# Kernel optimization log

Measured on AMD Instinct MI355X. Metric: run time of the kernel, lower is better.

The kernel has to match this reference:

```python
import jax, jax.numpy as jnp
import numpy as np

EPS = 1e-12  # F.normalize eps


def _gather_nb(var, idx):
    # var: [B, N, C], idx: [B, N, K] -> [B, N, K, C]; out[b,n,k,c] = var[b, idx[b,n,k], c]
    return jnp.take_along_axis(var[:, :, None, :], idx[:, :, :, None], axis=1)


def _l2norm(v):
    n = jnp.sqrt(jnp.sum(v * v, axis=-1, keepdims=True))
    return v / jnp.maximum(n, EPS)


def setup_inputs() -> dict:
    key = jax.random.key(0)
    ks = jax.random.split(key, 16)
    B, N, K, dim, hid = 4, 4096, 16, 128, 64
    s = 0.05
    return {
        "pos": jax.random.normal(ks[0], (B, N, 3), jnp.float32),
        "x": jax.random.normal(ks[1], (B, dim, N), jnp.float32),
        "idx": jax.random.randint(ks[2], (B, N, K), 0, N, jnp.int64),
        "dist": jax.random.uniform(ks[3], (B, N, K), jnp.float32),
        "W_qkv": jax.random.normal(ks[4], (3 * dim, dim), jnp.float32) * s,
        "W1": jax.random.normal(ks[5], (hid, 10), jnp.float32) * s,
        "b1": jax.random.normal(ks[6], (hid,), jnp.float32) * s,
        "W2": jax.random.normal(ks[7], (dim, hid), jnp.float32) * s,
        "b2": jax.random.normal(ks[8], (dim,), jnp.float32) * s,
        "Wm1": jax.random.normal(ks[9], (4 * dim, dim), jnp.float32) * s,
        "bm1": jax.random.normal(ks[10], (4 * dim,), jnp.float32) * s,
        "Wm2": jax.random.normal(ks[11], (dim, 4 * dim), jnp.float32) * s,
        "bm2": jax.random.normal(ks[12], (dim,), jnp.float32) * s,
    }


def reference(pos, x, idx, dist, W_qkv, W1, b1, W2, b2, Wm1, bm1, Wm2, bm2):
    B, _, N = x.shape
    xt = jnp.transpose(x, (0, 2, 1))                      # [B, N, C]
    qkv = xt @ W_qkv.T                                    # [B, N, 3C]
    Q, K_, V = jnp.split(qkv, 3, axis=-1)

    Qg = _gather_nb(Q, idx)                               # [B, N, K, C]
    Kg = _gather_nb(K_, idx)
    Vg = _gather_nb(V, idx)

    # position embedding: [center(3) | neighbor(3) | diff(3) | dist(1)] -> MLP 10->hid->C
    pos_nb = _gather_nb(pos, idx)                         # [B, N, K, 3]
    pos_c = jnp.broadcast_to(pos[:, :, None, :], pos_nb.shape)
    feat10 = jnp.concatenate(
        [pos_c, pos_nb, pos_c - pos_nb, dist[..., None]], axis=-1)  # [B, N, K, 10]
    pos_emb = jax.nn.relu(feat10 @ W1.T + b1) @ W2.T + b2  # [B, N, K, C]

    Knorm = _l2norm(Kg + pos_emb)                         # [B, N, K, C]
    Vrel = jax.nn.relu(Vg + pos_emb)                      # [B, N, K, C]
    Qn = _l2norm(Qg)                                      # [B, N, K, C]

    # kv_context: contract over N per neighbor slot k -> [B, K, C, C]
    kv = jnp.einsum('bnkc,bnkd->bkcd', Knorm, Vrel)
    # (1/N) Qn @ kv, then sum over k -> [B, N, C]
    agg = jnp.einsum('bnkc,bkcd->bnd', Qn, kv) / N

    out = jax.nn.relu(agg @ Wm1.T + bm1) @ Wm2.T + bm2 + xt  # [B, N, C]
    return jnp.transpose(out, (0, 2, 1))                     # [B, C, N]
```

## Files before the change

### kernel.cpp

```cpp
#include <hip/hip_runtime.h>
#include <math.h>

#define Bn 4
#define Nn 4096
#define Kn 16
#define Cn 128
#define HIDn 64

#define OFF_WQKVBF 0
#define OFF_WM1BF  24576
#define OFF_WM2BF  57344
#define OFF_W2BFG  90112
#define OFF_QNBF   95232
#define OFF_KMBF   1143808
#define OFF_VMBF   2192384
#define OFF_KVT32  3240960
#define OFF_KVTBF  4289536
#define OFF_AGG0   4813824
#define OFF_AGG1   6910976
#define OFF_FLAG   9008128

typedef short bf16x8 __attribute__((ext_vector_type(8)));
typedef float f32x4 __attribute__((ext_vector_type(4)));

__device__ inline unsigned short f2bf(float f) {
  union { float f; unsigned u; } v; v.f = f;
  unsigned r = v.u + 0x7fffu + ((v.u >> 16) & 1u);
  return (unsigned short)(r >> 16);
}
__device__ inline float b2f(unsigned short s) {
  union { unsigned u; float f; } v; v.u = ((unsigned)s) << 16; return v.f;
}

__global__ void k0_prep(const float* __restrict__ Wqkv,
                        const float* __restrict__ Wm1, const float* __restrict__ Wm2,
                        const float* __restrict__ W2,
                        const int* __restrict__ idx_raw, float* ws) {
  if (blockIdx.x == 0 && threadIdx.x == 0) {
    int any = 0;
    for (int i = 0; i < 64; ++i) any |= idx_raw[2 * i + 1];
    ((int*)(ws + OFF_FLAG))[0] = (any == 0) ? 1 : 0;
  }
  int t = blockIdx.x * 256 + threadIdx.x;
  if (t < 49152) { ((unsigned short*)(ws + OFF_WQKVBF))[t] = f2bf(Wqkv[t]); return; }
  t -= 49152;
  if (t < 65536) { ((unsigned short*)(ws + OFF_WM1BF))[t] = f2bf(Wm1[t]); return; }
  t -= 65536;
  if (t < 65536) { ((unsigned short*)(ws + OFF_WM2BF))[t] = f2bf(Wm2[t]); return; }
  t -= 65536;
  if (t < 8192) { ((unsigned short*)(ws + OFF_W2BFG))[t] = f2bf(W2[t]); return; }
}

__global__ __launch_bounds__(256, 2) void k1_qkv(const float* __restrict__ x, float* ws) {
  __shared__ __align__(16) unsigned short a_lds[32 * 136];
  __shared__ __align__(16) float qkv_lds[32 * 388];
  const unsigned short* Wq = (const unsigned short*)(ws + OFF_WQKVBF);
  unsigned short* Qnbf = (unsigned short*)(ws + OFF_QNBF);
  unsigned short* KmBF = (unsigned short*)(ws + OFF_KMBF);
  unsigned short* VmBF = (unsigned short*)(ws + OFF_VMBF);
  int b = blockIdx.x >> 7;
  int n0 = (blockIdx.x & 127) << 5;
  int t = threadIdx.x;
  int w = t >> 6, l = t & 63, ml = l & 15, gq = l >> 4;
#pragma unroll
  for (int i = 0; i < 16; ++i) {
    int id = t + 256 * i;
    int c = id >> 5, j = id & 31;
    a_lds[j * 136 + c] = f2bf(x[(b * Cn + c) * Nn + n0 + j]);
  }
  __syncthreads();
  f32x4 acc[2][6];
#pragma unroll
  for (int i = 0; i < 2; ++i)
#pragma unroll
    for (int j = 0; j < 6; ++j) acc[i][j] = (f32x4)0.f;
#pragma unroll
  for (int kc = 0; kc < 4; ++kc) {
    bf16x8 av0 = *(const bf16x8*)&a_lds[ml * 136 + kc * 32 + 8 * gq];
    bf16x8 av1 = *(const bf16x8*)&a_lds[(ml + 16) * 136 + kc * 32 + 8 * gq];
#pragma unroll
    for (int nf = 0; nf < 6; ++nf) {
      int m = 96 * w + 16 * nf + ml;
      bf16x8 bv = *(const bf16x8*)&Wq[m * 128 + kc * 32 + 8 * gq];
      acc[0][nf] = __builtin_amdgcn_mfma_f32_16x16x32_bf16(av0, bv, acc[0][nf], 0, 0, 0);
      acc[1][nf] = __builtin_amdgcn_mfma_f32_16x16x32_bf16(av1, bv, acc[1][nf], 0, 0, 0);
    }
  }
#pragma unroll
  for (int mf = 0; mf < 2; ++mf)
#pragma unroll
    for (int nf = 0; nf < 6; ++nf)
#pragma unroll
      for (int r = 0; r < 4; ++r)
        qkv_lds[(16 * mf + 4 * gq + r) * 388 + 96 * w + 16 * nf + ml] = acc[mf][nf][r];
  __syncthreads();
  {
    int g = t >> 3, l8 = t & 7;
    float4 q4[4];
    float ss = 0.f;
#pragma unroll
    for (int q = 0; q < 4; ++q) {
      q4[q] = *(const float4*)&qkv_lds[g * 388 + l8 * 16 + 4 * q];
      ss = fmaf(q4[q].x, q4[q].x, ss); ss = fmaf(q4[q].y, q4[q].y, ss);
      ss = fmaf(q4[q].z, q4[q].z, ss); ss = fmaf(q4[q].w, q4[q].w, ss);
    }
    ss += __shfl_xor(ss, 1); ss += __shfl_xor(ss, 2); ss += __shfl_xor(ss, 4);
    float sc = 1.f / fmaxf(sqrtf(ss), 1e-12f);
    union { unsigned short us[8]; uint4 u4; } o0, o1;
#pragma unroll
    for (int q = 0; q < 2; ++q) {
      o0.us[q * 4 + 0] = f2bf(q4[q].x * sc); o0.us[q * 4 + 1] = f2bf(q4[q].y * sc);
      o0.us[q * 4 + 2] = f2bf(q4[q].z * sc); o0.us[q * 4 + 3] = f2bf(q4[q].w * sc);
    }
#pragma unroll
    for (int q = 0; q < 2; ++q) {
      o1.us[q * 4 + 0] = f2bf(q4[2 + q].x * sc); o1.us[q * 4 + 1] = f2bf(q4[2 + q].y * sc);
      o1.us[q * 4 + 2] = f2bf(q4[2 + q].z * sc); o1.us[q * 4 + 3] = f2bf(q4[2 + q].w * sc);
    }
    *(uint4*)&Qnbf[(b * Nn + n0 + g) * Cn + l8 * 16] = o0.u4;
    *(uint4*)&Qnbf[(b * Nn + n0 + g) * Cn + l8 * 16 + 8] = o1.u4;
  }
#pragma unroll
  for (int i = 0; i < 2; ++i) {
    int id = t + 256 * i;
    int row = id >> 4, c8 = id & 15;
    const float* kp = &qkv_lds[row * 388 + 128 + c8 * 8];
    const float* vp = &qkv_lds[row * 388 + 256 + c8 * 8];
    union { unsigned short us[8]; uint4 u4; } ko, vo;
#pragma unroll
    for (int j = 0; j < 8; ++j) { ko.us[j] = f2bf(kp[j]); vo.us[j] = f2bf(vp[j]); }
    *(uint4*)&KmBF[(b * Nn + n0 + row) * Cn + c8 * 8] = ko.u4;
    *(uint4*)&VmBF[(b * Nn + n0 + row) * Cn + c8 * 8] = vo.u4;
  }
}

#define CH2 8
__global__ __launch_bounds__(256, 2) void k2_kv(const float* __restrict__ pos,
                                                const float* __restrict__ dist,
                                                const int* __restrict__ idxp,
                                                const float* __restrict__ W1,
                                                const float* __restrict__ b1,
                                                const float* __restrict__ b2,
                                                float* ws) {
  __shared__ __align__(16) unsigned short h_lds[32 * 72];
  __shared__ __align__(16) unsigned short pe_bf[32 * 136];
  __shared__ __align__(16) unsigned short K_rm[32 * 136];
  __shared__ __align__(16) unsigned short V_rm[32 * 136];
  __shared__ __align__(16) unsigned short KnT[2][128 * 40];
  __shared__ __align__(16) unsigned short VrT[2][128 * 40];

  const unsigned short* KmBF = (const unsigned short*)(ws + OFF_KMBF);
  const unsigned short* VmBF = (const unsigned short*)(ws + OFF_VMBF);
  const unsigned short* W2g = (const unsigned short*)(ws + OFF_W2BFG);
  float* kvt = ws + OFF_KVT32;
  int flag = ((const int*)(ws + OFF_FLAG))[0];

  int bid = blockIdx.x;
  int b = bid & 3;
  int rest = bid >> 2;
  int k = rest & 15, ch = rest >> 4;
  int t = threadIdx.x;
  int w = t >> 6, l = t & 63;
  int ml = l & 15, gq = l >> 4;

  int g = t >> 3, l8 = t & 7;
  int nl = (t >> 3) & 7, half = t & 7;
  int n_b2 = 8 * w + nl;
  int side = t >> 7, cc = t & 127;

  float b2v0 = b2[32 * w + ml];
  float b2v1 = b2[32 * w + 16 + ml];

  f32x4 acc[2][8];
#pragma unroll
  for (int i = 0; i < 2; ++i)
#pragma unroll
    for (int j = 0; j < 8; ++j) acc[i][j] = (f32x4)0.f;

  int nbase = ch * 512;
  union U8 { unsigned short us[8]; uint4 u4; };

  int fidx_m = (b * Nn + nbase + g) * Kn + k;
  int jn_m = flag ? idxp[2 * fidx_m] : idxp[fidx_m];
  float dd = dist[fidx_m];
  float pc0 = pos[(b * Nn + nbase + g) * 3 + 0];
  float pc1 = pos[(b * Nn + nbase + g) * 3 + 1];
  float pc2 = pos[(b * Nn + nbase + g) * 3 + 2];
  float pn0 = pos[(b * Nn + jn_m) * 3 + 0];
  float pn1 = pos[(b * Nn + jn_m) * 3 + 1];
  float pn2 = pos[(b * Nn + jn_m) * 3 + 2];
  int fidx_b = (b * Nn + nbase + n_b2) * Kn + k;
  int jn_b = flag ? idxp[2 * fidx_b] : idxp[fidx_b];
  U8 ka, kb, va, vb;
  {
    const unsigned short* krow = &KmBF[(b * Nn + jn_b) * Cn];
    const unsigned short* vrow = &VmBF[(b * Nn + jn_b) * Cn];
    ka.u4 = *(const uint4*)&krow[half * 16];
    kb.u4 = *(const uint4*)&krow[half * 16 + 8];
    va.u4 = *(const uint4*)&vrow[half * 16];
    vb.u4 = *(const uint4*)&vrow[half * 16 + 8];
  }

  for (int it = 0; it < 16; ++it) {
    {
      float f10[10] = {pc0, pc1, pc2, pn0, pn1, pn2, pc0 - pn0, pc1 - pn1, pc2 - pn2, dd};
      union { unsigned short us[8]; uint4 u4; } hv;
#pragma unroll
      for (int oo = 0; oo < 8; ++oo) {
        int o = l8 * 8 + oo;
        float a = b1[o];
#pragma unroll
        for (int i2 = 0; i2 < 10; ++i2) a = fmaf(W1[o * 10 + i2], f10[i2], a);
        hv.us[oo] = f2bf(fmaxf(a, 0.f));
      }
      *(uint4*)&h_lds[g * 72 + l8 * 8] = hv.u4;
    }
    int itn = (it < 15) ? it + 1 : 15;
    int n0n = nbase + itn * 32;
    int fidx_mn = (b * Nn + n0n + g) * Kn + k;
    int jn_mn = flag ? idxp[2 * fidx_mn] : idxp[fidx_mn];
    float ddn = dist[fidx_mn];
    int fidx_bn = (b * Nn + n0n + n_b2) * Kn + k;
    int jn_bn = flag ? idxp[2 * fidx_bn] : idxp[fidx_bn];
    __syncthreads();
    if (it > 0) {
      const unsigned short* ktp = KnT[(it - 1) & 1];
      const unsigned short* vtp = VrT[(it - 1) & 1];
      bf16x8 av[2];
#pragma unroll
      for (int mf = 0; mf < 2; ++mf)
        av[mf] = *(const bf16x8*)&vtp[(32 * w + 16 * mf + ml) * 40 + 8 * gq];
#pragma unroll
      for (int nf = 0; nf < 8; ++nf) {
        bf16x8 bv = *(const bf16x8*)&ktp[(16 * nf + ml) * 40 + 8 * gq];
#pragma unroll
        for (int mf = 0; mf < 2; ++mf)
          acc[mf][nf] = __builtin_amdgcn_mfma_f32_16x16x32_bf16(av[mf], bv, acc[mf][nf], 0, 0, 0);
      }
    }
    {
      f32x4 pacc[2][2];
#pragma unroll
      for (int i = 0; i < 2; ++i)
#pragma unroll
        for (int j = 0; j < 2; ++j) pacc[i][j] = (f32x4)0.f;
#pragma unroll
      for (int hc = 0; hc < 64; hc += 32) {
        bf16x8 av[2];
#pragma unroll
        for (int mf = 0; mf < 2; ++mf)
          av[mf] = *(const bf16x8*)&h_lds[(ml + 16 * mf) * 72 + hc + 8 * gq];
#pragma unroll
        for (int nf = 0; nf < 2; ++nf) {
          int c = 32 * w + 16 * nf + ml;
          bf16x8 bv = *(const bf16x8*)&W2g[c * 64 + hc + 8 * gq];
          pacc[0][nf] = __builtin_amdgcn_mfma_f32_16x16x32_bf16(av[0], bv, pacc[0][nf], 0, 0, 0);
          pacc[1][nf] = __builtin_amdgcn_mfma_f32_16x16x32_bf16(av[1], bv, pacc[1][nf], 0, 0, 0);
        }
      }
#pragma unroll
      for (int mf = 0; mf < 2; ++mf)
#pragma unroll
        for (int nf = 0; nf < 2; ++nf) {
          int c = 32 * w + 16 * nf + ml;
          float bias = nf ? b2v1 : b2v0;
#pragma unroll
          for (int r = 0; r < 4; ++r)
            pe_bf[(16 * mf + 4 * gq + r) * 136 + c] = f2bf(pacc[mf][nf][r] + bias);
        }
    }
    __syncthreads();
    {
      U8 pa, pb;
      pa.u4 = *(const uint4*)&pe_bf[n_b2 * 136 + half * 16];
      pb.u4 = *(const uint4*)&pe_bf[n_b2 * 136 + half * 16 + 8];
      float kr[16], vr[16];
      float ss = 0.f;
#pragma unroll
      for (int j = 0; j < 16; ++j) {
        float pe = b2f((j < 8) ? pa.us[j] : pb.us[j - 8]);
        float kg = b2f((j < 8) ? ka.us[j] : kb.us[j - 8]);
        float vg = b2f((j < 8) ? va.us[j] : vb.us[j - 8]);
        kr[j] = kg + pe;
        vr[j] = fmaxf(vg + pe, 0.f);
        ss = fmaf(kr[j], kr[j], ss);
      }
      ss += __shfl_xor(ss, 1); ss += __shfl_xor(ss, 2); ss += __shfl_xor(ss, 4);
      float sc = 1.f / fmaxf(sqrtf(ss), 1e-12f);
      union { unsigned short us[8]; uint4 u4; } o;
#pragma unroll
      for (int hh = 0; hh < 2; ++hh) {
#pragma unroll
        for (int j = 0; j < 8; ++j) o.us[j] = f2bf(kr[hh * 8 + j] * sc);
        *(uint4*)&K_rm[n_b2 * 136 + half * 16 + 8 * hh] = o.u4;
      }
#pragma unroll
      for (int hh = 0; hh < 2; ++hh) {
#pragma unroll
        for (int j = 0; j < 8; ++j) o.us[j] = f2bf(vr[hh * 8 + j]);
        *(uint4*)&V_rm[n_b2 * 136 + half * 16 + 8 * hh] = o.u4;
      }
    }
    float pc0n = pos[(b * Nn + n0n + g) * 3 + 0];
    float pc1n = pos[(b * Nn + n0n + g) * 3 + 1];
    float pc2n = pos[(b * Nn + n0n + g) * 3 + 2];
    float pn0n = pos[(b * Nn + jn_mn) * 3 + 0];
    float pn1n = pos[(b * Nn + jn_mn) * 3 + 1];
    float pn2n = pos[(b * Nn + jn_mn) * 3 + 2];
    U8 kan, kbn, van, vbn;
    {
      const unsigned short* krow = &KmBF[(b * Nn + jn_bn) * Cn];
      const unsigned short* vrow = &VmBF[(b * Nn + jn_bn) * Cn];
      kan.u4 = *(const uint4*)&krow[half * 16];
      kbn.u4 = *(const uint4*)&krow[half * 16 + 8];
      van.u4 = *(const uint4*)&vrow[half * 16];
      vbn.u4 = *(const uint4*)&vrow[half * 16 + 8];
    }
    __syncthreads();
    {
      const unsigned short* src = side ? V_rm : K_rm;
      unsigned short* dst = side ? VrT[it & 1] : KnT[it & 1];
      unsigned v[16];
#pragma unroll
      for (int i = 0; i < 16; ++i) {
        unsigned lo = src[(2 * i) * 136 + cc];
        unsigned hi = src[(2 * i + 1) * 136 + cc];
        v[i] = lo | (hi << 16);
      }
#pragma unroll
      for (int i = 0; i < 4; ++i) {
        uint4 pk = {v[4 * i], v[4 * i + 1], v[4 * i + 2], v[4 * i + 3]};
        *(uint4*)&dst[cc * 40 + 8 * i] = pk;
      }
    }
    dd = ddn;
    pc0 = pc0n; pc1 = pc1n; pc2 = pc2n;
    pn0 = pn0n; pn1 = pn1n; pn2 = pn2n;
    ka.u4 = kan.u4; kb.u4 = kbn.u4; va.u4 = van.u4; vb.u4 = vbn.u4;
  }
  __syncthreads();
  {
    const unsigned short* ktp = KnT[15 & 1];
    const unsigned short* vtp = VrT[15 & 1];
    bf16x8 av[2];
#pragma unroll
    for (int mf = 0; mf < 2; ++mf)
      av[mf] = *(const bf16x8*)&vtp[(32 * w + 16 * mf + ml) * 40 + 8 * gq];
#pragma unroll
    for (int nf = 0; nf < 8; ++nf) {
      bf16x8 bv = *(const bf16x8*)&ktp[(16 * nf + ml) * 40 + 8 * gq];
#pragma unroll
      for (int mf = 0; mf < 2; ++mf)
        acc[mf][nf] = __builtin_amdgcn_mfma_f32_16x16x32_bf16(av[mf], bv, acc[mf][nf], 0, 0, 0);
    }
  }
  float* kvp = kvt + (b * Kn + k) * Cn * Cn;
#pragma unroll
  for (int mf = 0; mf < 2; ++mf)
#pragma unroll
    for (int nf = 0; nf < 8; ++nf) {
      int c = 16 * nf + ml;
#pragma unroll
      for (int r = 0; r < 4; ++r) {
        int d = 32 * w + 16 * mf + 4 * gq + r;
        atomicAdd(&kvp[d * Cn + c], acc[mf][nf][r]);
      }
    }
}

__global__ __launch_bounds__(256) void k2b_cvt(float* ws) {
  const float* src = ws + OFF_KVT32;
  unsigned short* dst = (unsigned short*)(ws + OFF_KVTBF);
  int i = blockIdx.x * 256 + threadIdx.x;
  float4 a = *(const float4*)&src[i * 8];
  float4 c = *(const float4*)&src[i * 8 + 4];
  union { unsigned short us[8]; uint4 u4; } o;
  o.us[0] = f2bf(a.x); o.us[1] = f2bf(a.y); o.us[2] = f2bf(a.z); o.us[3] = f2bf(a.w);
  o.us[4] = f2bf(c.x); o.us[5] = f2bf(c.y); o.us[6] = f2bf(c.z); o.us[7] = f2bf(c.w);
  *(uint4*)&dst[i * 8] = o.u4;
}

__global__ __launch_bounds__(256, 4) void k3_agg(const int* __restrict__ idxp, float* ws) {
  __shared__ __align__(16) unsigned short qt[32 * 136];
  const unsigned short* Qnbf = (const unsigned short*)(ws + OFF_QNBF);
  const unsigned short* kvtbf = (const unsigned short*)(ws + OFF_KVTBF);
  int flag = ((const int*)(ws + OFF_FLAG))[0];

  int bid = blockIdx.x;
  int b = bid & 3;
  int kh = (bid >> 2) & 1;
  int nt = bid >> 3;
  int n0 = nt * 32;
  int t = threadIdx.x;
  int w = t >> 6, l = t & 63;
  int ml = l & 15, gq = l >> 4;

  f32x4 acc[2][2];
#pragma unroll
  for (int i = 0; i < 2; ++i)
#pragma unroll
    for (int j = 0; j < 2; ++j) acc[i][j] = (f32x4)0.f;

  for (int kk = 0; kk < 8; ++kk) {
    int k = kh * 8 + kk;
    __syncthreads();
#pragma unroll
    for (int i = 0; i < 2; ++i) {
      int id = t + 256 * i;
      int row = id >> 4, c16 = id & 15;
      int fidx = (b * Nn + n0 + row) * Kn + k;
      int jn = flag ? idxp[2 * fidx] : idxp[fidx];
      uint4 v = *(const uint4*)&Qnbf[(b * Nn + jn) * Cn + c16 * 8];
      *(uint4*)&qt[row * 136 + c16 * 8] = v;
    }
    __syncthreads();
    const unsigned short* kvp = &kvtbf[(b * Kn + k) * Cn * Cn];
#pragma unroll
    for (int c0 = 0; c0 < 128; c0 += 32) {
      bf16x8 a0 = *(const bf16x8*)&qt[ml * 136 + c0 + 8 * gq];
      bf16x8 a1 = *(const bf16x8*)&qt[(ml + 16) * 136 + c0 + 8 * gq];
#pragma unroll
      for (int nf = 0; nf < 2; ++nf) {
        int d = 32 * w + 16 * nf + ml;
        bf16x8 bv = *(const bf16x8*)&kvp[d * Cn + c0 + 8 * gq];
        acc[0][nf] = __builtin_amdgcn_mfma_f32_16x16x32_bf16(a0, bv, acc[0][nf], 0, 0, 0);
        acc[1][nf] = __builtin_amdgcn_mfma_f32_16x16x32_bf16(a1, bv, acc[1][nf], 0, 0, 0);
      }
    }
  }
  float* ag = ws + (kh ? OFF_AGG1 : OFF_AGG0);
#pragma unroll
  for (int mf = 0; mf < 2; ++mf)
#pragma unroll
    for (int nf = 0; nf < 2; ++nf) {
      int d = 32 * w + 16 * nf + ml;
#pragma unroll
      for (int r = 0; r < 4; ++r) {
        int n = n0 + 16 * mf + 4 * gq + r;
        ag[(b * Nn + n) * Cn + d] = acc[mf][nf][r];
      }
    }
}

__global__ __launch_bounds__(256, 2) void k4_mlp(const float* __restrict__ x,
                                                 const float* __restrict__ bm1,
                                                 const float* __restrict__ bm2,
                                                 float* __restrict__ out, float* ws) {
  __shared__ __align__(16) unsigned short a_lds[32 * 136];
  __shared__ __align__(16) unsigned short h_lds[32 * 520];
  __shared__ float out_s[128 * 33];
  const float* agg0 = ws + OFF_AGG0;
  const float* agg1 = ws + OFF_AGG1;
  const unsigned short* Wm1bf = (const unsigned short*)(ws + OFF_WM1BF);
  const unsigned short* Wm2bf = (const unsigned short*)(ws + OFF_WM2BF);
  const float invN = 1.f / (float)Nn;
  int b = blockIdx.x >> 7;
  int n0 = (blockIdx.x & 127) << 5;
  int t = threadIdx.x;
  int w = t >> 6, l = t & 63, ml = l & 15, gq = l >> 4;
#pragma unroll
  for (int i = 0; i < 4; ++i) {
    int id = t + 256 * i;
    int row = id >> 5, c4 = id & 31;
    int off = (b * Nn + n0 + row) * Cn + c4 * 4;
    float4 v0 = *(const float4*)&agg0[off];
    float4 v1 = *(const float4*)&agg1[off];
    union { unsigned short us[4]; uint2 u2; } o;
    o.us[0] = f2bf((v0.x + v1.x) * invN); o.us[1] = f2bf((v0.y + v1.y) * invN);
    o.us[2] = f2bf((v0.z + v1.z) * invN); o.us[3] = f2bf((v0.w + v1.w) * invN);
    *(uint2*)&a_lds[row * 136 + c4 * 4] = o.u2;
  }
  __syncthreads();
  {
    f32x4 hacc[2][8];
#pragma unroll
    for (int i = 0; i < 2; ++i)
#pragma unroll
      for (int j = 0; j < 8; ++j) hacc[i][j] = (f32x4)0.f;
#pragma unroll
    for (int kc = 0; kc < 4; ++kc) {
      bf16x8 av0 = *(const bf16x8*)&a_lds[ml * 136 + kc * 32 + 8 * gq];
      bf16x8 av1 = *(const bf16x8*)&a_lds[(ml + 16) * 136 + kc * 32 + 8 * gq];
#pragma unroll
      for (int nf = 0; nf < 8; ++nf) {
        int h = 128 * w + 16 * nf + ml;
        bf16x8 bv = *(const bf16x8*)&Wm1bf[h * 128 + kc * 32 + 8 * gq];
        hacc[0][nf] = __builtin_amdgcn_mfma_f32_16x16x32_bf16(av0, bv, hacc[0][nf], 0, 0, 0);
        hacc[1][nf] = __builtin_amdgcn_mfma_f32_16x16x32_bf16(av1, bv, hacc[1][nf], 0, 0, 0);
      }
    }
#pragma unroll
    for (int mf = 0; mf < 2; ++mf)
#pragma unroll
      for (int nf = 0; nf < 8; ++nf) {
        int h = 128 * w + 16 * nf + ml;
        float bias = bm1[h];
#pragma unroll
        for (int r = 0; r < 4; ++r)
          h_lds[(16 * mf + 4 * gq + r) * 520 + h] = f2bf(fmaxf(hacc[mf][nf][r] + bias, 0.f));
      }
  }
  __syncthreads();
  {
    f32x4 oacc[2][2];
#pragma unroll
    for (int i = 0; i < 2; ++i)
#pragma unroll
      for (int j = 0; j < 2; ++j) oacc[i][j] = (f32x4)0.f;
#pragma unroll
    for (int kc = 0; kc < 16; ++kc) {
      bf16x8 av0 = *(const bf16x8*)&h_lds[ml * 520 + kc * 32 + 8 * gq];
      bf16x8 av1 = *(const bf16x8*)&h_lds[(ml + 16) * 520 + kc * 32 + 8 * gq];
#pragma unroll
      for (int nf = 0; nf < 2; ++nf) {
        int co = 32 * w + 16 * nf + ml;
        bf16x8 bv = *(const bf16x8*)&Wm2bf[co * 512 + kc * 32 + 8 * gq];
        oacc[0][nf] = __builtin_amdgcn_mfma_f32_16x16x32_bf16(av0, bv, oacc[0][nf], 0, 0, 0);
        oacc[1][nf] = __builtin_amdgcn_mfma_f32_16x16x32_bf16(av1, bv, oacc[1][nf], 0, 0, 0);
      }
    }
#pragma unroll
    for (int mf = 0; mf < 2; ++mf)
#pragma unroll
      for (int nf = 0; nf < 2; ++nf) {
        int co = 32 * w + 16 * nf + ml;
        float bias = bm2[co];
#pragma unroll
        for (int r = 0; r < 4; ++r)
          out_s[co * 33 + 16 * mf + 4 * gq + r] = oacc[mf][nf][r] + bias;
      }
  }
  __syncthreads();
#pragma unroll
  for (int i = 0; i < 16; ++i) {
    int id = t + 256 * i;
    int co = id >> 5, j = id & 31;
    out[(b * Cn + co) * Nn + n0 + j] = out_s[co * 33 + j] + x[(b * Cn + co) * Nn + n0 + j];
  }
}

extern "C" void kernel_launch(void* const* d_in, const int* in_sizes, int n_in,
                              void* d_out, int out_size, void* d_ws, size_t ws_size,
                              hipStream_t stream) {
  const float* pos  = (const float*)d_in[0];
  const float* x    = (const float*)d_in[1];
  const int*   idx  = (const int*)d_in[2];
  const float* dist = (const float*)d_in[3];
  const float* Wqkv = (const float*)d_in[4];
  const float* W1   = (const float*)d_in[5];
  const float* b1   = (const float*)d_in[6];
  const float* W2   = (const float*)d_in[7];
  const float* b2   = (const float*)d_in[8];
  const float* Wm1  = (const float*)d_in[9];
  const float* bm1  = (const float*)d_in[10];
  const float* Wm2  = (const float*)d_in[11];
  const float* bm2  = (const float*)d_in[12];
  float* out = (float*)d_out;
  float* ws = (float*)d_ws;

  hipMemsetAsync(ws + OFF_KVT32, 0, (size_t)Bn * Kn * Cn * Cn * sizeof(float), stream);
  hipLaunchKernelGGL(k0_prep, dim3(736), dim3(256), 0, stream, Wqkv, Wm1, Wm2, W2, idx, ws);
  hipLaunchKernelGGL(k1_qkv, dim3(Bn * 128), dim3(256), 0, stream, x, ws);
  hipLaunchKernelGGL(k2_kv, dim3(Bn * Kn * CH2), dim3(256), 0, stream, pos, dist, idx, W1, b1, b2, ws);
  hipLaunchKernelGGL(k2b_cvt, dim3(512), dim3(256), 0, stream, ws);
  hipLaunchKernelGGL(k3_agg, dim3(Bn * 2 * 128), dim3(256), 0, stream, idx, ws);
  hipLaunchKernelGGL(k4_mlp, dim3(Bn * 128), dim3(256), 0, stream, x, bm1, bm2, out, ws);
}
```

Before: 160.3 us.

## Write K/V tiles directly into transposed swizzled LDS, drop transpose pass

The k2_kv loop now writes the normalized K and relu'd V values straight into the transposed KnT/VrT buffers using an XOR-swizzled column index, and the MFMA operand loads apply the matching swizzle. This removes the row-major K_rm/V_rm staging buffers, one __syncthreads per iteration and the separate transpose pass. The position embedding is kept in fp32 LDS instead of bf16, which avoids a round-trip conversion but uses more LDS. The trade-off is many scalar 2-byte LDS stores in place of vectorized 16-byte ones, which may cause bank conflicts.

```diff
diff --git a/kernel.cpp b/kernel.cpp
--- a/kernel.cpp
+++ b/kernel.cpp
@@ -143,9 +143,7 @@
                                                 const float* __restrict__ b2,
                                                 float* ws) {
   __shared__ __align__(16) unsigned short h_lds[32 * 72];
-  __shared__ __align__(16) unsigned short pe_bf[32 * 136];
-  __shared__ __align__(16) unsigned short K_rm[32 * 136];
-  __shared__ __align__(16) unsigned short V_rm[32 * 136];
+  __shared__ __align__(16) float pe_lds[32 * 132];
   __shared__ __align__(16) unsigned short KnT[2][128 * 40];
   __shared__ __align__(16) unsigned short VrT[2][128 * 40];
 
@@ -166,7 +164,7 @@
   int g = t >> 3, l8 = t & 7;
   int nl = (t >> 3) & 7, half = t & 7;
   int n_b2 = 8 * w + nl;
-  int side = t >> 7, cc = t & 127;
+  int swb = ((w ^ (half & 3)) << 3) + nl;
 
   float b2v0 = b2[32 * w + ml];
   float b2v1 = b2[32 * w + 16 + ml];
@@ -228,11 +226,16 @@
       const unsigned short* vtp = VrT[(it - 1) & 1];
       bf16x8 av[2];
 #pragma unroll
-      for (int mf = 0; mf < 2; ++mf)
-        av[mf] = *(const bf16x8*)&vtp[(32 * w + 16 * mf + ml) * 40 + 8 * gq];
+      for (int mf = 0; mf < 2; ++mf) {
+        int d = 32 * w + 16 * mf + ml;
+        int blk = gq ^ ((2 * w + mf) & 3);
+        av[mf] = *(const bf16x8*)&vtp[d * 40 + 8 * blk];
+      }
 #pragma unroll
       for (int nf = 0; nf < 8; ++nf) {
-        bf16x8 bv = *(const bf16x8*)&ktp[(16 * nf + ml) * 40 + 8 * gq];
+        int c = 16 * nf + ml;
+        int blk = gq ^ (nf & 3);
+        bf16x8 bv = *(const bf16x8*)&ktp[c * 40 + 8 * blk];
 #pragma unroll
         for (int mf = 0; mf < 2; ++mf)
           acc[mf][nf] = __builtin_amdgcn_mfma_f32_16x16x32_bf16(av[mf], bv, acc[mf][nf], 0, 0, 0);
@@ -266,40 +269,35 @@
           float bias = nf ? b2v1 : b2v0;
 #pragma unroll
           for (int r = 0; r < 4; ++r)
-            pe_bf[(16 * mf + 4 * gq + r) * 136 + c] = f2bf(pacc[mf][nf][r] + bias);
+            pe_lds[(16 * mf + 4 * gq + r) * 132 + c] = pacc[mf][nf][r] + bias;
         }
     }
     __syncthreads();
     {
-      U8 pa, pb;
-      pa.u4 = *(const uint4*)&pe_bf[n_b2 * 136 + half * 16];
-      pb.u4 = *(const uint4*)&pe_bf[n_b2 * 136 + half * 16 + 8];
-      float kr[16], vr[16];
+      float p[16];
+#pragma unroll
+      for (int q = 0; q < 4; ++q) {
+        float4 p4 = *(const float4*)&pe_lds[n_b2 * 132 + half * 16 + 4 * q];
+        p[4 * q] = p4.x; p[4 * q + 1] = p4.y; p[4 * q + 2] = p4.z; p[4 * q + 3] = p4.w;
+      }
+      unsigned short* kdst = KnT[it & 1];
+      unsigned short* vdst = VrT[it & 1];
+      float kr[16];
       float ss = 0.f;
 #pragma unroll
       for (int j = 0; j < 16; ++j) {
-        float pe = b2f((j < 8) ? pa.us[j] : pb.us[j - 8]);
         float kg = b2f((j < 8) ? ka.us[j] : kb.us[j - 8]);
         float vg = b2f((j < 8) ? va.us[j] : vb.us[j - 8]);
-        kr[j] = kg + pe;
-        vr[j] = fmaxf(vg + pe, 0.f);
+        kr[j] = kg + p[j];
+        float vv = fmaxf(vg + p[j], 0.f);
         ss = fmaf(kr[j], kr[j], ss);
+        vdst[(half * 16 + j) * 40 + swb] = f2bf(vv);
       }
       ss += __shfl_xor(ss, 1); ss += __shfl_xor(ss, 2); ss += __shfl_xor(ss, 4);
       float sc = 1.f / fmaxf(sqrtf(ss), 1e-12f);
-      union { unsigned short us[8]; uint4 u4; } o;
-#pragma unroll
-      for (int hh = 0; hh < 2; ++hh) {
-#pragma unroll
-        for (int j = 0; j < 8; ++j) o.us[j] = f2bf(kr[hh * 8 + j] * sc);
-        *(uint4*)&K_rm[n_b2 * 136 + half * 16 + 8 * hh] = o.u4;
-      }
-#pragma unroll
-      for (int hh = 0; hh < 2; ++hh) {
-#pragma unroll
-        for (int j = 0; j < 8; ++j) o.us[j] = f2bf(vr[hh * 8 + j]);
-        *(uint4*)&V_rm[n_b2 * 136 + half * 16 + 8 * hh] = o.u4;
-      }
+#pragma unroll
+      for (int j = 0; j < 16; ++j)
+        kdst[(half * 16 + j) * 40 + swb] = f2bf(kr[j] * sc);
     }
     float pc0n = pos[(b * Nn + n0n + g) * 3 + 0];
     float pc1n = pos[(b * Nn + n0n + g) * 3 + 1];
@@ -316,23 +314,6 @@
       van.u4 = *(const uint4*)&vrow[half * 16];
       vbn.u4 = *(const uint4*)&vrow[half * 16 + 8];
     }
-    __syncthreads();
-    {
-      const unsigned short* src = side ? V_rm : K_rm;
-      unsigned short* dst = side ? VrT[it & 1] : KnT[it & 1];
-      unsigned v[16];
-#pragma unroll
-      for (int i = 0; i < 16; ++i) {
-        unsigned lo = src[(2 * i) * 136 + cc];
-        unsigned hi = src[(2 * i + 1) * 136 + cc];
-        v[i] = lo | (hi << 16);
-      }
-#pragma unroll
-      for (int i = 0; i < 4; ++i) {
-        uint4 pk = {v[4 * i], v[4 * i + 1], v[4 * i + 2], v[4 * i + 3]};
-        *(uint4*)&dst[cc * 40 + 8 * i] = pk;
-      }
-    }
     dd = ddn;
     pc0 = pc0n; pc1 = pc1n; pc2 = pc2n;
     pn0 = pn0n; pn1 = pn1n; pn2 = pn2n;
@@ -344,11 +325,16 @@
     const unsigned short* vtp = VrT[15 & 1];
     bf16x8 av[2];
 #pragma unroll
-    for (int mf = 0; mf < 2; ++mf)
-      av[mf] = *(const bf16x8*)&vtp[(32 * w + 16 * mf + ml) * 40 + 8 * gq];
+    for (int mf = 0; mf < 2; ++mf) {
+      int d = 32 * w + 16 * mf + ml;
+      int blk = gq ^ ((2 * w + mf) & 3);
+      av[mf] = *(const bf16x8*)&vtp[d * 40 + 8 * blk];
+    }
 #pragma unroll
     for (int nf = 0; nf < 8; ++nf) {
-      bf16x8 bv = *(const bf16x8*)&ktp[(16 * nf + ml) * 40 + 8 * gq];
+      int c = 16 * nf + ml;
+      int blk = gq ^ (nf & 3);
+      bf16x8 bv = *(const bf16x8*)&ktp[c * 40 + 8 * blk];
 #pragma unroll
       for (int mf = 0; mf < 2; ++mf)
         acc[mf][nf] = __builtin_amdgcn_mfma_f32_16x16x32_bf16(av[mf], bv, acc[mf][nf], 0, 0, 0);
```

After: 152.6 us. 4.8% less time.
